# Kernel optimization log

Hardware: AMD Instinct MI355X
Metric: run time of the kernel (lower is better)

Reference implementation:

```python
import jax, jax.numpy as jnp
import numpy as np

SR = 16000; NFFT = 1024; HOP = 256; NMELS = 80; GRUH = 256; ZDIM = 16
NBINS = 65; HID = 512; B = 8; TLEN = 160000; PAD = NFFT // 2; IRLEN = 8000

def _consts():
    freqs = np.linspace(0, SR / 2, NFFT // 2 + 1); fsq = freqs ** 2
    aw = (12194.217 ** 2 * fsq ** 2) / ((fsq + 20.6 ** 2) * (fsq + 107.7 ** 2) * (fsq + 737.9 ** 2) * (fsq + 12194.217 ** 2) ** 0.5 + 1e-8)
    h2m = lambda f: 2595.0 * np.log10(1.0 + f / 700.0)
    m2h = lambda m: 700.0 * (10.0 ** (m / 2595.0) - 1.0)
    f_pts = m2h(np.linspace(h2m(0.0), h2m(SR / 2.0), NMELS + 2))
    fd = f_pts[1:] - f_pts[:-1]
    sl = f_pts[None, :] - freqs[:, None]
    fb = np.maximum(0.0, np.minimum(-sl[:, :-2] / fd[:-1], sl[:, 2:] / fd[1:]))
    win = 0.5 - 0.5 * np.cos(2.0 * np.pi * np.arange(NFFT) / NFFT)  # periodic hann
    return jnp.asarray(aw, jnp.float32), jnp.asarray(fb, jnp.float32), jnp.asarray(win, jnp.float32)
AW, MELFB, WIN = _consts()

def _frame(x, size, hop):
    n = (x.shape[-1] - size) // hop + 1
    idx = jnp.arange(n)[:, None] * hop + jnp.arange(size)[None, :]
    return x[:, idx]

def _stft(x):  # [B,T] -> [B, n_frames, 513] complex
    xp = jnp.pad(x, ((0, 0), (PAD, PAD)), mode='reflect')
    return jnp.fft.rfft(_frame(xp, NFFT, HOP) * WIN, axis=-1)

def _istft(spec, length):  # [B, n_frames, 513] -> [B, length]
    fr = jnp.fft.irfft(spec, n=NFFT, axis=-1) * WIN
    n = fr.shape[1]; total = (n - 1) * HOP + NFFT
    idx = (jnp.arange(n)[:, None] * HOP + jnp.arange(NFFT)[None, :]).reshape(-1)
    out = jnp.zeros((fr.shape[0], total), fr.dtype).at[:, idx].add(fr.reshape(fr.shape[0], -1))
    wsq = jnp.zeros((total,), WIN.dtype).at[idx].add(jnp.tile(WIN ** 2, (n,)))
    out = out / jnp.where(wsq > 1e-11, wsq, 1.0)
    return out[:, PAD:PAD + length]

def _lin_interp(x, size):  # torch F.interpolate(mode='linear', align_corners=False) on last axis
    L = x.shape[-1]
    pos = jnp.clip((jnp.arange(size) + 0.5) * (L / size) - 0.5, 0.0, L - 1.0)
    lo = jnp.floor(pos).astype(jnp.int32); hi = jnp.minimum(lo + 1, L - 1); w = pos - lo
    return x[..., lo] * (1.0 - w) + x[..., hi] * w

def _gru(x, wih, whh, bih, bhh):  # torch nn.GRU, batch_first, h0=0
    xp = x @ wih.T + bih
    def step(h, xt):
        gh = h @ whh.T + bhh
        xr, xz, xn = jnp.split(xt, 3, -1); hr, hz, hn = jnp.split(gh, 3, -1)
        r = jax.nn.sigmoid(xr + hr); z = jax.nn.sigmoid(xz + hz)
        nn_ = jnp.tanh(xn + r * hn)
        h = (1.0 - z) * nn_ + z * h
        return h, h
    h0 = jnp.zeros((x.shape[0], whh.shape[1]), x.dtype)
    _, hs = jax.lax.scan(step, h0, jnp.swapaxes(xp, 0, 1))
    return jnp.swapaxes(hs, 0, 1)

def _forward(audio, gender, age, gru_wih, gru_whh, gru_bih, gru_bhh, proj_w, proj_b,
             w0, b0, g0, e0, w1, b1, g1, e1, w2, b2, g2, e2,
             oq_w, oq_b, vt_w, vt_b, nf_w, nf_b, ir):
    # --- pitch via autocorrelation ---
    xp = jnp.pad(audio, ((0, 0), (PAD, PAD)), mode='reflect')
    fr = _frame(xp, NFFT, HOP)
    ps = jnp.abs(jnp.fft.rfft(fr, n=2 * NFFT, axis=-1)) ** 2
    ac = jnp.fft.irfft(ps, n=2 * NFFT, axis=-1)[..., :NFFT]
    ac = ac / (ac[..., :1] + 1e-8)
    min_lag, max_lag = SR // 1000, SR // 50  # 16, 320
    reg = ac[..., min_lag:max_lag]
    mv = jnp.max(reg, -1); mi = jnp.argmax(reg, -1)
    f0 = SR / (mi.astype(jnp.float32) + min_lag + 1e-8)
    f0 = jnp.where(mv < 0.3, 0.0, f0)[..., None]  # [B,F,1]
    # --- loudness + mels ---
    spec = jnp.abs(_stft(audio)) ** 2  # [B,F,513]
    loud = 10.0 * jnp.log10(jnp.mean((spec + 1e-8) * AW, -1, keepdims=True))  # [B,F,1]
    mels = jnp.log(spec @ MELFB + 1e-5)  # [B,F,80]
    mels = (mels - mels.mean(1, keepdims=True)) / jnp.sqrt(mels.var(1, keepdims=True) + 1e-5)
    z = _gru(mels, gru_wih, gru_whh, gru_bih, gru_bhh) @ proj_w.T + proj_b  # [B,F,16]
    Fn = f0.shape[1]
    # --- controller ---
    gb = jnp.broadcast_to(gender[:, None, :], (gender.shape[0], Fn, 2))
    ab = jnp.broadcast_to(age[:, None, :], (age.shape[0], Fn, 1))
    h = jnp.concatenate([z, (jnp.log(f0 + 1e-5) - 4.0) / 4.0, loud / 100.0 + 1.0, gb, ab], -1)
    for W, bb, gm, bt in ((w0, b0, g0, e0), (w1, b1, g1, e1), (w2, b2, g2, e2)):
        h = h @ W.T + bb
        h = (h - h.mean(-1, keepdims=True)) / jnp.sqrt(h.var(-1, keepdims=True) + 1e-5) * gm + bt
        h = jnp.where(h >= 0, h, 0.1 * h)  # LeakyReLU(0.1)
    oq = jax.nn.sigmoid(h @ oq_w.T + oq_b)
    vt = jax.nn.sigmoid(h @ vt_w.T + vt_b)
    nf = jax.nn.sigmoid(h @ nf_w.T + nf_b)
    amp = 10.0 ** (loud / 20.0)
    # --- decoder ---
    L = audio.shape[-1]
    f0u = _lin_interp(f0[..., 0], L); ampu = _lin_interp(amp[..., 0], L); oqu = _lin_interp(oq[..., 0], L)
    phase = jnp.cumsum(f0u / SR, -1); p = phase - jnp.floor(phase)
    oqc = jnp.clip(oqu, 0.1, 0.9)
    pulse = 0.5 * (1.0 - jnp.cos(jnp.pi * p / (oqc + 1e-8)))
    g = pulse * jax.nn.sigmoid((oqc - p) * 100.0)
    glottal = jnp.pad(g[..., 1:] - g[..., :-1], ((0, 0), (1, 0)))
    noise = jax.random.normal(jax.random.key(42), glottal.shape, glottal.dtype)
    def apply_filter(ex, filt):
        es = _stft(ex)  # [B,nf,513]
        ft = _lin_interp(jnp.swapaxes(filt, 1, 2), es.shape[1])  # time interp
        ff = _lin_interp(jnp.swapaxes(ft, 1, 2), es.shape[2])    # bin interp 65->513
        return _istft(es * ff, L)
    dry = (apply_filter(glottal, vt) + apply_filter(noise, nf)) * ampu
    # --- FFT reverb ---
    nconv = int(2 ** int(np.ceil(np.log2(L + IRLEN - 1))))
    wet = jnp.fft.irfft(jnp.fft.rfft(dry, n=nconv) * jnp.fft.rfft(ir, n=nconv), n=nconv)[..., :L]
    return wet, dry

def setup_inputs() -> dict:
    ks = iter(jax.random.split(jax.random.key(0), 48))
    def nrm(shape, s=0.05):
        return jax.random.normal(next(ks), shape, jnp.float32) * s
    inp = {}
    inp['audio'] = jax.random.normal(next(ks), (B, TLEN), jnp.float32)
    inp['gender'] = jax.random.uniform(next(ks), (B, 2), jnp.float32)
    inp['age'] = jax.random.uniform(next(ks), (B, 1), jnp.float32)
    inp['gru_wih'] = nrm((3 * GRUH, NMELS)); inp['gru_whh'] = nrm((3 * GRUH, GRUH))
    inp['gru_bih'] = jnp.zeros((3 * GRUH,), jnp.float32); inp['gru_bhh'] = jnp.zeros((3 * GRUH,), jnp.float32)
    inp['proj_w'] = nrm((ZDIM, GRUH)); inp['proj_b'] = jnp.zeros((ZDIM,), jnp.float32)
    din = ZDIM + 5
    inp['w0'] = nrm((HID, din)); inp['b0'] = jnp.zeros((HID,), jnp.float32)
    inp['g0'] = jnp.ones((HID,), jnp.float32); inp['e0'] = jnp.zeros((HID,), jnp.float32)
    inp['w1'] = nrm((HID, HID)); inp['b1'] = jnp.zeros((HID,), jnp.float32)
    inp['g1'] = jnp.ones((HID,), jnp.float32); inp['e1'] = jnp.zeros((HID,), jnp.float32)
    inp['w2'] = nrm((HID, HID)); inp['b2'] = jnp.zeros((HID,), jnp.float32)
    inp['g2'] = jnp.ones((HID,), jnp.float32); inp['e2'] = jnp.zeros((HID,), jnp.float32)
    inp['oq_w'] = nrm((1, HID)); inp['oq_b'] = jnp.zeros((1,), jnp.float32)
    inp['vt_w'] = nrm((NBINS, HID)); inp['vt_b'] = jnp.zeros((NBINS,), jnp.float32)
    inp['nf_w'] = nrm((NBINS, HID)); inp['nf_b'] = jnp.zeros((NBINS,), jnp.float32)
    decay = jnp.exp(-jnp.linspace(0.0, 5.0, IRLEN))
    inp['ir'] = jax.random.normal(next(ks), (IRLEN,), jnp.float32) * 0.1 * decay
    return inp

def reference(audio, gender, age, gru_wih, gru_whh, gru_bih, gru_bhh, proj_w, proj_b,
              w0, b0, g0, e0, w1, b1, g1, e1, w2, b2, g2, e2,
              oq_w, oq_b, vt_w, vt_b, nf_w, nf_b, ir):
    return _forward(audio, gender, age, gru_wih, gru_whh, gru_bih, gru_bhh, proj_w, proj_b,
                    w0, b0, g0, e0, w1, b1, g1, e1, w2, b2, g2, e2,
                    oq_w, oq_b, vt_w, vt_b, nf_w, nf_b, ir)
```

## Files before the change

### kernel.cpp

```cpp
#include <hip/hip_runtime.h>
#include <math.h>

#define SRF 16000.0f
#define HOP 256
#define FRM 626
#define BB 8
#define TLEN 160000
#define NFRM (BB*FRM)
#define NCONV 262144
#define ACCLEN 161024
#define GCH 40

constexpr size_t oWIN   = 0;
constexpr size_t oTW    = oWIN + 1024;
constexpr size_t oDIAG  = oTW + 1024;
constexpr size_t oTWF   = oDIAG + 16;
constexpr size_t oTWC   = oTWF + 1024;
constexpr size_t oAW    = oTWC + 1024;
constexpr size_t oMELFB = oAW + 513;
constexpr size_t oWSQI  = oMELFB + 513*80;
constexpr size_t oWIHT  = oWSQI + ACCLEN;
constexpr size_t oW0T   = oWIHT + 80*768;
constexpr size_t oW1T   = oW0T + 21*512;
constexpr size_t oW2T   = oW1T + 512*512;
constexpr size_t oVTT   = oW2T + 512*512;
constexpr size_t oNFT   = oVTT + 512*65;
constexpr size_t oF0    = oNFT + 512*65;
constexpr size_t oLOUD  = oF0 + NFRM;
constexpr size_t oOQ    = oLOUD + NFRM;
constexpr size_t oVT    = oOQ + NFRM;
constexpr size_t oNF    = oVT + (size_t)NFRM*65;
constexpr size_t oGLOT  = oNF + (size_t)NFRM*65;
constexpr size_t oNOISE = oGLOT + (size_t)BB*TLEN;
constexpr size_t oACC   = oNOISE + (size_t)BB*TLEN;
constexpr size_t oCONVA = oACC + (size_t)BB*ACCLEN;
constexpr size_t oEND   = oCONVA + (size_t)5*NCONV*2;
constexpr size_t oXP    = oEND;
constexpr size_t oGSUM  = oXP + (size_t)FRM*768*8;
constexpr size_t oGPRE  = oGSUM + 320;
constexpr size_t oEND2  = oGPRE + 640;
constexpr size_t oCONVB = oWSQI;
constexpr size_t oMEL = oCONVA;
constexpr size_t oHS  = oMEL + (size_t)NFRM*80;

constexpr long R_WIN=1024, R_TW=512, R_TWF=512, R_TWC=512, R_AW=513, R_MELFB=41040,
  R_WSQI=161024, R_WIHT=61440, R_W0T=10752, R_W1T=262144, R_W2T=262144,
  R_VTT=33280, R_NFT=33280, R_IR=NCONV;
constexpr long INIT_TOTAL = R_WIN+R_TW+R_TWF+R_TWC+R_AW+R_MELFB+R_WSQI+R_WIHT+R_W0T+
  R_W1T+R_W2T+R_VTT+R_NFT+R_IR;

constexpr int NOISEB = 313;
constexpr int ZACCB  = 315;
constexpr int MEGA_BLOCKS = 1 + NFRM + NOISEB + ZACCB;

typedef float f32x4 __attribute__((ext_vector_type(4)));
typedef __bf16 bf16x8 __attribute__((ext_vector_type(8)));
typedef short short8 __attribute__((ext_vector_type(8)));
#define MFMA_BF16 __builtin_amdgcn_mfma_f32_16x16x32_bf16

__device__ inline int mirror_idx(int j) {
  if (j < 0) j = -j;
  if (j >= TLEN) j = 2*TLEN - 2 - j;
  return j;
}
__device__ inline float sigm(float x) { return 1.0f/(1.0f + expf(-x)); }
__device__ inline unsigned short f2bf(float x) {
  unsigned u = __float_as_uint(x);
  return (unsigned short)((u + 0x7FFFu + ((u >> 16) & 1u)) >> 16);
}
__device__ inline float tanh_fast(float x) {
  return 1.0f - 2.0f/(__expf(2.0f*x) + 1.0f);
}

__device__ inline float interpF(const float* v, int i) {
  float pos = ((float)i + 0.5f) * (626.0f/160000.0f) - 0.5f;
  pos = fminf(fmaxf(pos, 0.0f), 625.0f);
  int lo = (int)floorf(pos);
  int hi = min(lo + 1, 625);
  float w = pos - (float)lo;
  return v[lo]*(1.0f - w) + v[hi]*w;
}
__device__ inline float interp65(const float* v, int k) {
  float pos = ((float)k + 0.5f) * (65.0f/513.0f) - 0.5f;
  pos = fminf(fmaxf(pos, 0.0f), 64.0f);
  int lo = (int)floorf(pos);
  int hi = min(lo + 1, 64);
  float w = pos - (float)lo;
  return v[lo]*(1.0f - w) + v[hi]*w;
}
__device__ inline float gwave(float ph, float oqu) {
  float p = ph - floorf(ph);
  float oqc = fminf(fmaxf(oqu, 0.1f), 0.9f);
  float pulse = 0.5f*(1.0f - cosf(3.14159265358979f * p / (oqc + 1e-8f)));
  float gs = 1.0f/(1.0f + __expf(-(oqc - p)*100.0f));
  return pulse*gs;
}

template<int LOGN, int TS>
__device__ inline void fft2(float2* c, const float2* tw, int tid, int nthr, bool inv) {
  constexpr int N = 1 << LOGN;
  for (int s = 1; s <= LOGN; ++s) {
    const int half = 1 << (s-1);
    const int tstep = (N >> s) * TS;
    for (int bf = tid; bf < (N>>1); bf += nthr) {
      int jj = bf & (half-1);
      int i0 = ((bf >> (s-1)) << s) + jj;
      int i1 = i0 + half;
      float2 wv = tw[jj*tstep];
      float wi = inv ? -wv.y : wv.y;
      float2 u = c[i0], v = c[i1];
      float tr  = v.x*wv.x - v.y*wi;
      float tci = v.x*wi  + v.y*wv.x;
      c[i0] = make_float2(u.x + tr, u.y + tci);
      c[i1] = make_float2(u.x - tr, u.y - tci);
    }
    __syncthreads();
  }
}

__device__ inline void threefry2x32(unsigned k0, unsigned k1, unsigned x0, unsigned x1,
                                    unsigned& o0, unsigned& o1) {
  unsigned ks2 = k0 ^ k1 ^ 0x1BD11BDAu;
  x0 += k0; x1 += k1;
#define TF_R(r) { x0 += x1; x1 = (x1<<(r)) | (x1>>(32-(r))); x1 ^= x0; }
  TF_R(13) TF_R(15) TF_R(26) TF_R(6)
  x0 += k1; x1 += ks2 + 1u;
  TF_R(17) TF_R(29) TF_R(16) TF_R(24)
  x0 += ks2; x1 += k0 + 2u;
  TF_R(13) TF_R(15) TF_R(26) TF_R(6)
  x0 += k0; x1 += k1 + 3u;
  TF_R(17) TF_R(29) TF_R(16) TF_R(24)
  x0 += k1; x1 += ks2 + 4u;
  TF_R(13) TF_R(15) TF_R(26) TF_R(6)
  x0 += ks2; x1 += k0 + 5u;
#undef TF_R
  o0 = x0; o1 = x1;
}

__device__ inline float erfinv_f(float x) {
  float w = -log1pf(-x*x);
  float p;
  if (w < 5.0f) {
    w = w - 2.5f;
    p = 2.81022636e-08f;
    p = fmaf(p, w, 3.43273939e-07f);
    p = fmaf(p, w, -3.5233877e-06f);
    p = fmaf(p, w, -4.39150654e-06f);
    p = fmaf(p, w, 0.00021858087f);
    p = fmaf(p, w, -0.00125372503f);
    p = fmaf(p, w, -0.00417768164f);
    p = fmaf(p, w, 0.246640727f);
    p = fmaf(p, w, 1.50140941f);
  } else {
    w = sqrtf(w) - 3.0f;
    p = -0.000200214257f;
    p = fmaf(p, w, 0.000100950558f);
    p = fmaf(p, w, 0.00134934322f);
    p = fmaf(p, w, -0.00367342844f);
    p = fmaf(p, w, 0.00573950773f);
    p = fmaf(p, w, -0.0076224613f);
    p = fmaf(p, w, 0.00943887047f);
    p = fmaf(p, w, 1.00167406f);
    p = fmaf(p, w, 2.83297682f);
  }
  return p*x;
}
__device__ inline float normal_from_bits(unsigned bits) {
  float f = __uint_as_float((bits >> 9) | 0x3F800000u) - 1.0f;
  float x = fmaxf(-0.99999994f, fmaf(f, 1.99999994f, -0.99999994f));
  return 1.41421356237f * erfinv_f(x);
}

__device__ inline double mel_fpt(int j) {
  double mmax = 2595.0 * log10(1.0 + 8000.0/700.0);
  return 700.0 * (pow(10.0, (mmax * (double)j / 81.0) / 2595.0) - 1.0);
}

__global__ void k_init(float* W, const float* wih, const float* w0,
                       const float* w1, const float* w2, const float* vtw, const float* nfw,
                       const float* ir) {
  long id = (long)blockIdx.x*256 + threadIdx.x;
  if (id < R_WIN) {
    double w = 0.5 - 0.5*cos(2.0*M_PI*(double)id/1024.0);
    W[oWIN+id] = (float)w; return;
  } id -= R_WIN;
  if (id < R_TW) {
    double a = -2.0*M_PI*(double)id/1024.0;
    W[oTW+2*id] = (float)cos(a); W[oTW+2*id+1] = (float)sin(a); return;
  } id -= R_TW;
  if (id < R_TWF) {
    double a = -2.0*M_PI*(double)id/262144.0;
    W[oTWF+2*id] = (float)cos(a); W[oTWF+2*id+1] = (float)sin(a); return;
  } id -= R_TWF;
  if (id < R_TWC) {
    double a = -2.0*M_PI*(double)id/512.0;
    W[oTWC+2*id] = (float)cos(a); W[oTWC+2*id+1] = (float)sin(a); return;
  } id -= R_TWC;
  if (id < R_AW) {
    double fr = (double)id*(8000.0/512.0); double fsq = fr*fr;
    double num = 12194.217*12194.217*fsq*fsq;
    double den = (fsq+20.6*20.6)*(fsq+107.7*107.7)*(fsq+737.9*737.9)*sqrt(fsq+12194.217*12194.217) + 1e-8;
    W[oAW+id] = (float)(num/den); return;
  } id -= R_AW;
  if (id < R_MELFB) {
    int k = (int)(id/80), m = (int)(id%80);
    double fk = (double)k*(8000.0/512.0);
    double f0p = mel_fpt(m), f1p = mel_fpt(m+1), f2p = mel_fpt(m+2);
    double lower = (fk - f0p)/(f1p - f0p);
    double upper = (f2p - fk)/(f2p - f1p);
    double v = fmax(0.0, fmin(lower, upper));
    W[oMELFB+id] = (float)v; return;
  } id -= R_MELFB;
  if (id < R_WSQI) {
    int t = (int)id;
    int n1 = t/256; if (n1 > 625) n1 = 625;
    int n0t = t - 1023 + 255; int n0 = (n0t > 0) ? n0t/256 : 0;
    double s = 0.0;
    for (int n = n0; n <= n1; ++n) {
      int o = t - n*256;
      double wv = 0.5 - 0.5*cos(2.0*M_PI*(double)o/1024.0);
      s += wv*wv;
    }
    float sf = (float)s;
    W[oWSQI+t] = (sf > 1e-11f) ? (1.0f/sf) : 1.0f; return;
  } id -= R_WSQI;
  if (id < R_WIHT) { long k = id/768, g = id%768; W[oWIHT+id] = wih[g*80+k];  return; } id -= R_WIHT;
  if (id < R_W0T)  { long d = id/512, j = id%512; W[oW0T+id] = w0[j*21+d];   return; } id -= R_W0T;
  if (id < R_W1T)  { long k = id/512, j = id%512; W[oW1T+id] = w1[j*512+k];  return; } id -= R_W1T;
  if (id < R_W2T)  { long k = id/512, j = id%512; W[oW2T+id] = w2[j*512+k];  return; } id -= R_W2T;
  if (id < R_VTT)  { long k = id/65,  m = id%65;  W[oVTT+id] = vtw[m*512+k]; return; } id -= R_VTT;
  if (id < R_NFT)  { long k = id/65,  m = id%65;  W[oNFT+id] = nfw[m*512+k]; return; } id -= R_NFT;
  if (id < R_IR) {
    size_t base = oCONVA + 2*((size_t)4*NCONV + id);
    W[base] = (id < 8000) ? ir[id] : 0.0f; W[base+1] = 0.0f; return;
  }
}

__global__ __launch_bounds__(256) void k_stft_mel(const float* audio, float* W) {
  int blk = blockIdx.x; int b = blk/FRM, f = blk%FRM; int tid = threadIdx.x;
  __shared__ float2 cb[1024];
  __shared__ float spec[513];
  __shared__ float redbuf[4];
  const float* arow = audio + (size_t)b*TLEN;
  const float2* tw = (const float2*)(W + oTW);
  for (int i = tid; i < 1024; i += 256) {
    float v = arow[mirror_idx(f*256 + i - 512)] * W[oWIN + i];
    int pos = __brev((unsigned)i) >> 22;
    cb[pos] = make_float2(v, 0.f);
  }
  __syncthreads();
  fft2<10,1>(cb, tw, tid, 256, false);
  for (int k = tid; k < 513; k += 256) { float2 z = cb[k]; spec[k] = z.x*z.x + z.y*z.y; }
  __syncthreads();
  float part = 0.f;
  for (int k = tid; k < 513; k += 256) part += (spec[k] + 1e-8f) * W[oAW + k];
  for (int off = 32; off; off >>= 1) part += __shfl_down(part, off, 64);
  if ((tid & 63) == 0) redbuf[tid >> 6] = part;
  __syncthreads();
  if (tid == 0) {
    float s = redbuf[0]+redbuf[1]+redbuf[2]+redbuf[3];
    W[oLOUD + blk] = 10.0f * log10f(s / 513.0f);
  }
  for (int m = tid; m < 80; m += 256) {
    double f0p = mel_fpt(m), f2p = mel_fpt(m + 2);
    int klo = (int)(f0p * (512.0/8000.0)); if (klo < 0) klo = 0;
    int khi = (int)(f2p * (512.0/8000.0)) + 1; if (khi > 512) khi = 512;
    float s = 0.f;
    for (int k = klo; k <= khi; ++k) s += spec[k]*W[oMELFB + (size_t)k*80 + m];
    W[oMEL + (size_t)blk*80 + m] = logf(s + 1e-5f);
  }
}

__global__ void k_melnorm(float* W) {
  int id = blockIdx.x*256 + threadIdx.x;
  if (id >= BB*80) return;
  int b = id/80, m = id%80;
  double s = 0.0, ss = 0.0;
  for (int f = 0; f < FRM; ++f) {
    double v = W[oMEL + ((size_t)b*FRM + f)*80 + m];
    s += v; ss += v*v;
  }
  double mean = s/FRM;
  double var = ss/FRM - mean*mean;
  float mu = (float)mean;
  float rstd = (float)(1.0/sqrt(var + 1e-5));
  for (int f = 0; f < FRM; ++f) {
    size_t idx = oMEL + ((size_t)b*FRM + f)*80 + m;
    W[idx] = (W[idx] - mu)*rstd;
  }
}

__global__ void k_xp(float* W, const float* bih) {
  size_t id = (size_t)blockIdx.x*256 + threadIdx.x;
  if (id >= (size_t)FRM*768*8) return;
  int b = (int)(id & 7);
  int g = (int)((id >> 3) % 768);
  int t = (int)(id / (768*8));
  const float* mrow = W + oMEL + ((size_t)b*FRM + t)*80;
  float acc = bih[g];
  for (int k = 0; k < 80; ++k) acc = fmaf(mrow[k], W[oWIHT + (size_t)k*768 + g], acc);
  W[oXP + id] = acc;
}

__global__ __launch_bounds__(512, 2) void k_mega(float* W, const float* audio,
                                                 const float* whh, const float* bhh) {
  __shared__ unsigned short sB[32768];
  __shared__ unsigned short sA[4096];
  __shared__ float sGT[9216];
  __shared__ float fr4[4][1032];
  __shared__ float wpow[8];
  __shared__ float wmax[8];
  __shared__ int   wmaxi[8];
  int tid = threadIdx.x;
  int blk = blockIdx.x;

  if (blk == 0) {
    int w = tid >> 6, l = tid & 63;
    const float* XP = W + oXP;
    float* HS = W + oHS;

    for (int idx = tid; idx < 32768; idx += 512) {
      int lcol = idx >> 8, k = idx & 255;
      int gcol = 96*(lcol >> 4) + 80 + (lcol & 15);
      sB[lcol*256 + (k ^ ((lcol & 7) << 3))] = f2bf(whh[(size_t)gcol*256 + k]);
    }
    for (int idx = tid; idx < 4096; idx += 512) sA[idx] = 0;

    int cl = l & 15, khalf = (l >> 4) * 8;
    bf16x8 bw[40];
    #pragma unroll
    for (int t2 = 0; t2 < 5; ++t2) {
      int col = 96*w + 16*t2 + cl;
      #pragma unroll
      for (int kk = 0; kk < 8; ++kk) {
        const float* src = whh + (size_t)col*256 + kk*32 + khalf;
        short8 tmp;
        #pragma unroll
        for (int j = 0; j < 8; ++j) tmp[j] = (short)f2bf(src[j]);
        bw[t2*8 + kk] = __builtin_bit_cast(bf16x8, tmp);
      }
    }

    int g = tid & 255, bbase = tid >> 8;
    float bh_r = bhh[g], bh_z = bhh[256 + g], bh_n = bhh[512 + g];
    float hprev[4] = {0.f, 0.f, 0.f, 0.f};
    int aXor = (cl & 7) << 3;
    int lcol5 = w*16 + cl;
    int rowg = l >> 4;
    int colb = 96*w + cl;
    int gtw = colb*12 + rowg*4;
    size_t xpr = (size_t)g*8 + 4*bbase;
    size_t xpz = (size_t)(256 + g)*8 + 4*bbase;
    size_t xpn = (size_t)(512 + g)*8 + 4*bbase;
    int gtr0 = g*12 + 4*bbase;
    int gtr1 = (256 + g)*12 + 4*bbase;
    int gtr2 = (512 + g)*12 + 4*bbase;

    __syncthreads();

#define LDA(kk) (*(const bf16x8*)&sA[(cl)*256 + (((kk)*32 + khalf) ^ aXor)])
#define LDB(kk) (*(const bf16x8*)&sB[(lcol5)*256 + (((kk)*32 + khalf) ^ aXor)])
#define STEPK(A_, kk) \
      c0 = MFMA_BF16(A_, bw[0*8+(kk)], c0, 0, 0, 0); \
      c1 = MFMA_BF16(A_, bw[1*8+(kk)], c1, 0, 0, 0); \
      c2 = MFMA_BF16(A_, bw[2*8+(kk)], c2, 0, 0, 0); \
      c3 = MFMA_BF16(A_, bw[3*8+(kk)], c3, 0, 0, 0); \
      c4 = MFMA_BF16(A_, bw[4*8+(kk)], c4, 0, 0, 0); \
      c5 = MFMA_BF16(A_, LDB(kk), c5, 0, 0, 0);

    for (int t = 0; t < FRM; ++t) {
      size_t xbase = (size_t)t*6144;
      float4 xr4 = *(const float4*)&XP[xbase + xpr];
      float4 xz4 = *(const float4*)&XP[xbase + xpz];
      float4 xn4 = *(const float4*)&XP[xbase + xpn];
      f32x4 c0 = {0,0,0,0}, c1 = {0,0,0,0}, c2 = {0,0,0,0};
      f32x4 c3 = {0,0,0,0}, c4 = {0,0,0,0}, c5 = {0,0,0,0};
      bf16x8 a0 = LDA(0), a1 = LDA(1), a2 = LDA(2), a3 = LDA(3);
      STEPK(a0, 0) STEPK(a1, 1) STEPK(a2, 2) STEPK(a3, 3)
      a0 = LDA(4); a1 = LDA(5); a2 = LDA(6); a3 = LDA(7);
      STEPK(a0, 4) STEPK(a1, 5) STEPK(a2, 6) STEPK(a3, 7)
      if (rowg < 3) {
        *(f32x4*)&sGT[gtw + 0*192]  = c0;
        *(f32x4*)&sGT[gtw + 1*192]  = c1;
        *(f32x4*)&sGT[gtw + 2*192]  = c2;
        *(f32x4*)&sGT[gtw + 3*192]  = c3;
        *(f32x4*)&sGT[gtw + 4*192]  = c4;
        *(f32x4*)&sGT[gtw + 5*192]  = c5;
      }
      __syncthreads();
      f32x4 rv = *(const f32x4*)&sGT[gtr0];
      f32x4 zv = *(const f32x4*)&sGT[gtr1];
      f32x4 nv = *(const f32x4*)&sGT[gtr2];
      #pragma unroll
      for (int j = 0; j < 4; ++j) {
        int bb = 4*bbase + j;
        float r = 1.0f/(1.0f + __expf(-(xr4[j] + rv[j] + bh_r)));
        float z = 1.0f/(1.0f + __expf(-(xz4[j] + zv[j] + bh_z)));
        float nn = tanh_fast(xn4[j] + r*(nv[j] + bh_n));
        float h = (1.0f - z)*nn + z*hprev[j];
        hprev[j] = h;
        HS[((size_t)bb*FRM + t)*256 + g] = h;
        sA[bb*256 + (g ^ ((bb & 7) << 3))] = f2bf(h);
      }
      __syncthreads();
    }
#undef LDA
#undef LDB
#undef STEPK
    return;
  }
  blk -= 1;

  if (blk < NFRM) {
    int b = blk/FRM, f = blk%FRM;
    const float* arow = audio + (size_t)b*TLEN;
    for (int idx = tid; idx < 4*1032; idx += 512) {
      int s = idx/1032, i = idx - s*1032;
      int j = i + s;
      fr4[s][i] = (j < 1024) ? arow[mirror_idx(f*256 + j - 512)] : 0.f;
    }
    __syncthreads();
    int lane = tid & 63, wv = tid >> 6;
    float p = 0.f;
    for (int i = tid; i < 1024; i += 512) { float x = fr4[0][i]; p += x*x; }
    for (int off = 32; off; off >>= 1) p += __shfl_down(p, off, 64);
    if (lane == 0) wpow[wv] = p;
    float vbest = -1e30f; int ibest = tid;
    if (tid < 304) {
      int lag = 16 + tid;
      int s = lag & 3, base = lag - s;
      int qmax = (1023 - lag) >> 2;
      float acc = 0.f;
      for (int q = 0; q <= qmax; ++q) {
        float4 u = *(const float4*)&fr4[0][4*q];
        float4 v = *(const float4*)&fr4[s][base + 4*q];
        acc += u.x*v.x + u.y*v.y + u.z*v.z + u.w*v.w;
      }
      vbest = acc;
    }
    for (int off = 32; off; off >>= 1) {
      float v2 = __shfl_down(vbest, off, 64);
      int i2 = __shfl_down(ibest, off, 64);
      if (v2 > vbest || (v2 == vbest && i2 < ibest)) { vbest = v2; ibest = i2; }
    }
    if (lane == 0) { wmax[wv] = vbest; wmaxi[wv] = ibest; }
    __syncthreads();
    if (tid == 0) {
      float ac0 = 0.f;
      #pragma unroll
      for (int q = 0; q < 8; ++q) ac0 += wpow[q];
      float bv = wmax[0]; int bi = wmaxi[0];
      #pragma unroll
      for (int q = 1; q < 8; ++q) {
        if (wmax[q] > bv || (wmax[q] == bv && wmaxi[q] < bi)) { bv = wmax[q]; bi = wmaxi[q]; }
      }
      float inv = 1.0f/(ac0 + 1e-8f);
      float best = bv*inv;
      W[oF0 + (size_t)blk] = (best < 0.3f) ? 0.0f : (SRF/(float)(bi + 16));
    }
    return;
  }
  blk -= NFRM;

  if (blk < NOISEB) {
    size_t base = (size_t)blk*4096;
    #pragma unroll
    for (int j = 0; j < 8; ++j) {
      size_t p = base + (size_t)j*512 + tid;
      if (p < (size_t)BB*TLEN) {
        unsigned o0, o1;
        threefry2x32(0u, 42u, 0u, (unsigned)p, o0, o1);
        W[oNOISE + p] = normal_from_bits(o0 ^ o1);
      }
    }
    return;
  }
  blk -= NOISEB;

  {
    size_t base = (size_t)blk*4096;
    #pragma unroll
    for (int j = 0; j < 8; ++j) {
      size_t p = base + (size_t)j*512 + tid;
      if (p < (size_t)BB*ACCLEN) W[oACC + p] = 0.0f;
    }
  }
}

__device__ inline void ln_lrelu(float acc[8], float gj, float ej, float out[8][512],
                                float wred[8][8][2], float stat[8][2],
                                int tid, int lane, int wv, int j) {
  #pragma unroll
  for (int i = 0; i < 8; ++i) {
    float s = acc[i], ss = acc[i]*acc[i];
    for (int off = 32; off; off >>= 1) { s += __shfl_down(s, off, 64); ss += __shfl_down(ss, off, 64); }
    if (lane == 0) { wred[i][wv][0] = s; wred[i][wv][1] = ss; }
  }
  __syncthreads();
  if (tid < 8) {
    float s = 0.f, ss = 0.f;
    #pragma unroll
    for (int w = 0; w < 8; ++w) { s += wred[tid][w][0]; ss += wred[tid][w][1]; }
    float mean = s/512.0f;
    float var = ss/512.0f - mean*mean;
    stat[tid][0] = mean;
    stat[tid][1] = 1.0f/sqrtf(var + 1e-5f);
  }
  __syncthreads();
  #pragma unroll
  for (int i = 0; i < 8; ++i) {
    float v = (acc[i] - stat[i][0])*stat[i][1]*gj + ej;
    out[i][j] = (v >= 0.f) ? v : 0.1f*v;
  }
}

__global__ __launch_bounds__(512) void k_mlp(float* W, const float* gender, const float* age,
    const float* projw, const float* projb,
    const float* b0, const float* g0, const float* e0,
    const float* b1, const float* g1, const float* e1,
    const float* b2, const float* g2, const float* e2,
    const float* oqw, const float* oqb, const float* vtb, const float* nfb) {
  __shared__ float hbuf[8][256];
  __shared__ float in0[8][21];
  __shared__ float actA[8][512];
  __shared__ float actB[8][512];
  __shared__ float wred[8][8][2];
  __shared__ float stat[8][2];
  int tid = threadIdx.x; int q0 = blockIdx.x*8;
  for (int x = tid; x < 2048; x += 512) {
    int i = x >> 8, k = x & 255;
    hbuf[i][k] = W[oHS + ((size_t)(q0 + i))*256 + k];
  }
  __syncthreads();
  if (tid < 128) {
    int i = tid >> 4, zi = tid & 15;
    float a = projb[zi];
    for (int k = 0; k < 256; ++k) a = fmaf(hbuf[i][k], projw[zi*256 + k], a);
    in0[i][zi] = a;
  } else if (tid < 168) {
    int x = tid - 128; int i = x/5, d = 16 + x%5;
    int q = q0 + i; int b = q/FRM;
    float v;
    if (d == 16) v = (logf(W[oF0 + q] + 1e-5f) - 4.0f)*0.25f;
    else if (d == 17) v = W[oLOUD + q]/100.0f + 1.0f;
    else if (d == 18) v = gender[b*2];
    else if (d == 19) v = gender[b*2 + 1];
    else v = age[b];
    in0[i][d] = v;
  }
  __syncthreads();
  int j = tid, lane = tid & 63, wv = tid >> 6;
  float acc[8];
  #pragma unroll
  for (int i = 0; i < 8; ++i) acc[i] = b0[j];
  for (int d = 0; d < 21; ++d) {
    float w = W[oW0T + (size_t)d*512 + j];
    #pragma unroll
    for (int i = 0; i < 8; ++i) acc[i] = fmaf(in0[i][d], w, acc[i]);
  }
  ln_lrelu(acc, g0[j], e0[j], actA, wred, stat, tid, lane, wv, j);
  __syncthreads();
  #pragma unroll
  for (int i = 0; i < 8; ++i) acc[i] = b1[j];
  for (int k = 0; k < 512; ++k) {
    float w = W[oW1T + (size_t)k*512 + j];
    #pragma unroll
    for (int i = 0; i < 8; ++i) acc[i] = fmaf(actA[i][k], w, acc[i]);
  }
  ln_lrelu(acc, g1[j], e1[j], actB, wred, stat, tid, lane, wv, j);
  __syncthreads();
  #pragma unroll
  for (int i = 0; i < 8; ++i) acc[i] = b2[j];
  for (int k = 0; k < 512; ++k) {
    float w = W[oW2T + (size_t)k*512 + j];
    #pragma unroll
    for (int i = 0; i < 8; ++i) acc[i] = fmaf(actB[i][k], w, acc[i]);
  }
  ln_lrelu(acc, g2[j], e2[j], actA, wred, stat, tid, lane, wv, j);
  __syncthreads();
  for (int x = tid; x < 520; x += 512) {
    int i = x/65, m = x%65;
    float a = vtb[m], a2 = nfb[m];
    for (int k = 0; k < 512; ++k) {
      float h = actA[i][k];
      a  = fmaf(h, W[oVTT + (size_t)k*65 + m], a);
      a2 = fmaf(h, W[oNFT + (size_t)k*65 + m], a2);
    }
    W[oVT + (size_t)(q0+i)*65 + m] = sigm(a);
    W[oNF + (size_t)(q0+i)*65 + m] = sigm(a2);
  }
  if (tid < 8) {
    float a = oqb[0];
    for (int k = 0; k < 512; ++k) a = fmaf(actA[tid][k], oqw[k], a);
    W[oOQ + q0 + tid] = sigm(a);
  }
}

__global__ __launch_bounds__(256) void k_gsum(float* W) {
  int blk = blockIdx.x; int b = blk/GCH, c = blk%GCH; int tid = threadIdx.x;
  __shared__ float ws[4];
  const float* f0r = W + oF0 + (size_t)b*FRM;
  int i0 = c*4096 + tid*16;
  float s = 0.f;
  #pragma unroll
  for (int j = 0; j < 16; ++j) {
    int i = i0 + j;
    if (i < TLEN) s += interpF(f0r, i)*(1.0f/SRF);
  }
  for (int off = 32; off; off >>= 1) s += __shfl_down(s, off, 64);
  if ((tid & 63) == 0) ws[tid >> 6] = s;
  __syncthreads();
  if (tid == 0) W[oGSUM + (size_t)b*GCH + c] = ws[0]+ws[1]+ws[2]+ws[3];
}

__global__ void k_gscan(float* W) {
  if (blockIdx.x == 0 && threadIdx.x == 0) {
    double* P = (double*)(W + oGPRE);
    for (int b = 0; b < BB; ++b) {
      double a = 0.0;
      for (int c = 0; c < GCH; ++c) {
        P[b*GCH + c] = a;
        a += (double)W[oGSUM + (size_t)b*GCH + c];
      }
    }
  }
}

__global__ __launch_bounds__(256) void k_gapply(float* W) {
  int blk = blockIdx.x; int b = blk/GCH, c = blk%GCH; int tid = threadIdx.x;
  __shared__ float wss[4];
  __shared__ float lastw[4];
  const float* f0r = W + oF0 + (size_t)b*FRM;
  const float* oqr = W + oOQ + (size_t)b*FRM;
  float* grow = W + oGLOT + (size_t)b*TLEN;
  double P = ((const double*)(W + oGPRE))[b*GCH + c];
  int i0 = c*4096 + tid*16;
  int lane = tid & 63, wv = tid >> 6;
  float v[16]; float ts = 0.f;
  #pragma unroll
  for (int j = 0; j < 16; ++j) {
    int i = i0 + j;
    float x = (i < TLEN) ? interpF(f0r, i)*(1.0f/SRF) : 0.f;
    v[j] = x; ts += x;
  }
  float sc = ts;
  #pragma unroll
  for (int off = 1; off < 64; off <<= 1) {
    float o = __shfl_up(sc, off, 64);
    if (lane >= off) sc += o;
  }
  if (lane == 63) wss[wv] = sc;
  __syncthreads();
  float wpre = 0.f;
  for (int q = 0; q < wv; ++q) wpre += wss[q];
  double ph0 = P + (double)(wpre + sc - ts);
  float run = 0.f; float gq[16];
  #pragma unroll
  for (int j = 0; j < 16; ++j) {
    int i = i0 + j;
    run += v[j];
    float ph = (float)(ph0 + (double)run);
    gq[j] = gwave(ph, interpF(oqr, min(i, TLEN-1)));
  }
  float prev = __shfl_up(gq[15], 1, 64);
  if (lane == 63) lastw[wv] = gq[15];
  __syncthreads();
  if (lane == 0) {
    if (wv > 0) prev = lastw[wv - 1];
    else if (i0 > 0) prev = gwave((float)P, interpF(oqr, i0 - 1));
    else prev = 0.f;
  }
  #pragma unroll
  for (int j = 0; j < 16; ++j) {
    int i = i0 + j;
    if (i < TLEN) {
      float gl = (j == 0) ? prev : gq[j-1];
      grow[i] = (i == 0) ? 0.f : (gq[j] - gl);
    }
  }
}

__global__ __launch_bounds__(256) void k_filtsynth(float* W) {
  int blk = blockIdx.x; int b = blk/FRM, f = blk%FRM; int tid = threadIdx.x;
  __shared__ float2 cZ[1024], cS[1024];
  __shared__ float fvt[65], fnf[65];
  const float* grow = W + oGLOT + (size_t)b*TLEN;
  const float* nrow = W + oNOISE + (size_t)b*TLEN;
  const float2* tw = (const float2*)(W + oTW);
  for (int i = tid; i < 1024; i += 256) {
    int si = mirror_idx(f*256 + i - 512);
    float wv = W[oWIN + i];
    int pos = __brev((unsigned)i) >> 22;
    cZ[pos] = make_float2(grow[si]*wv, nrow[si]*wv);
  }
  if (tid < 65) {
    fvt[tid] = W[oVT + ((size_t)b*FRM + f)*65 + tid];
    fnf[tid] = W[oNF + ((size_t)b*FRM + f)*65 + tid];
  }
  __syncthreads();
  fft2<10,1>(cZ, tw, tid, 256, false);
  for (int k = tid; k <= 512; k += 256) {
    int km = (1024 - k) & 1023;
    float2 z1 = cZ[k], z2 = cZ[km];
    float Gr = 0.5f*(z1.x + z2.x), Gi = 0.5f*(z1.y - z2.y);
    float Nr = 0.5f*(z1.y + z2.y), Ni = 0.5f*(z2.x - z1.x);
    float fv = interp65(fvt, k), fn = interp65(fnf, k);
    float Sr = Gr*fv + Nr*fn, Si = Gi*fv + Ni*fn;
    cS[__brev((unsigned)k) >> 22] = make_float2(Sr, Si);
    if (km != k) cS[__brev((unsigned)km) >> 22] = make_float2(Sr, -Si);
  }
  __syncthreads();
  fft2<10,1>(cS, tw, tid, 256, true);
  float* arow = W + oACC + (size_t)b*ACCLEN + (size_t)f*256;
  for (int i = tid; i < 1024; i += 256) {
    float xv = cS[i].x*(1.0f/1024.0f)*W[oWIN + i];
    atomicAdd(arow + i, xv);
  }
}

__global__ void k_dry(float* W, float* dout) {
  size_t id = (size_t)blockIdx.x*256 + threadIdx.x;
  if (id >= (size_t)4*NCONV) return;
  int t = (int)(id / NCONV);
  int n = (int)(id % NCONV);
  float dv0 = 0.f, dv1 = 0.f;
  if (n < TLEN) {
    float pos = ((float)n + 0.5f) * (626.0f/160000.0f) - 0.5f;
    pos = fminf(fmaxf(pos, 0.0f), 625.0f);
    int lo = (int)floorf(pos);
    int hi = min(lo + 1, 625);
    float wgt = pos - (float)lo;
    float wsq = W[oWSQI + 512 + n];
    #pragma unroll
    for (int q = 0; q < 2; ++q) {
      int b = 2*t + q;
      float val = W[oACC + (size_t)b*ACCLEN + 512 + n] * wsq;
      const float* lrow = W + oLOUD + (size_t)b*FRM;
      float a0 = exp10f(lrow[lo]*0.05f);
      float a1 = exp10f(lrow[hi]*0.05f);
      float dv = val*(a0*(1.0f - wgt) + a1*wgt);
      if (q == 0) dv0 = dv; else dv1 = dv;
      dout[(size_t)BB*TLEN + (size_t)b*TLEN + n] = dv;
    }
  }
  ((float2*)(W + oCONVA))[id] = make_float2(dv0, dv1);
}

__global__ __launch_bounds__(256) void k_conv_f1(const float* in, float* out,
                                                 const float* tw, const float* twf,
                                                 const float* twc) {
  int blk = blockIdx.x; int t = blk >> 9; int bcol = blk & 511; int tid = threadIdx.x;
  __shared__ float2 cb[512];
  const float2* src = (const float2*)in + (size_t)t*NCONV;
  for (int a = tid; a < 512; a += 256) {
    int pos = __brev((unsigned)a) >> 23;
    cb[pos] = src[(size_t)a*512 + bcol];
  }
  __syncthreads();
  fft2<9,2>(cb, (const float2*)tw, tid, 256, false);
  float2* dst = (float2*)out + (size_t)t*NCONV + (size_t)bcol*512;
  for (int k1 = tid; k1 < 512; k1 += 256) {
    unsigned m = (unsigned)bcol * (unsigned)k1;
    float2 tc = ((const float2*)twc)[m >> 9];
    float2 tf = ((const float2*)twf)[m & 511];
    float wr = tc.x*tf.x - tc.y*tf.y;
    float wi = tc.x*tf.y + tc.y*tf.x;
    float2 v = cb[k1];
    dst[k1] = make_float2(v.x*wr - v.y*wi, v.x*wi + v.y*wr);
  }
}

__global__ __launch_bounds__(256) void k_conv_f2(const float* in, float* out, const float* tw) {
  int blk = blockIdx.x; int t = blk >> 9; int k1 = blk & 511; int tid = threadIdx.x;
  __shared__ float2 cb[512];
  const float2* src = (const float2*)in + (size_t)t*NCONV;
  for (int bb2 = tid; bb2 < 512; bb2 += 256) {
    int pos = __brev((unsigned)bb2) >> 23;
    cb[pos] = src[(size_t)bb2*512 + k1];
  }
  __syncthreads();
  fft2<9,2>(cb, (const float2*)tw, tid, 256, false);
  float2* dst = (float2*)out + (size_t)t*NCONV;
  for (int k2 = tid; k2 < 512; k2 += 256) {
    dst[(size_t)k1 + 512*(size_t)k2] = cb[k2];
  }
}

__global__ __launch_bounds__(256) void k_conv_f2w(const float* in, float* dout, const float* tw) {
  int blk = blockIdx.x; int t = blk >> 9; int k1 = blk & 511; int tid = threadIdx.x;
  __shared__ float2 cb[512];
  const float2* src = (const float2*)in + (size_t)t*NCONV;
  for (int bb2 = tid; bb2 < 512; bb2 += 256) {
    int pos = __brev((unsigned)bb2) >> 23;
    cb[pos] = src[(size_t)bb2*512 + k1];
  }
  __syncthreads();
  fft2<9,2>(cb, (const float2*)tw, tid, 256, false);
  float* d0 = dout + (size_t)(2*t)*TLEN;
  float* d1 = dout + (size_t)(2*t + 1)*TLEN;
  for (int k2 = tid; k2 < 512; k2 += 256) {
    int n = k1 + 512*k2;
    if (n < TLEN) {
      float2 V = cb[k2];
      d0[n] = V.x * (1.0f/262144.0f);
      d1[n] = -V.y * (1.0f/262144.0f);
    }
  }
}

__global__ void k_mul(float* W) {
  constexpr size_t HALF = NCONV/2;
  size_t id = (size_t)blockIdx.x*256 + threadIdx.x;
  if (id >= (size_t)4*(HALF + 1)) return;
  int t = (int)(id / (HALF + 1));
  size_t k = id % (HALF + 1);
  size_t km = (NCONV - k) & (NCONV - 1);
  float2* A = (float2*)(W + oCONVA);
  float2 z1 = A[(size_t)t*NCONV + k];
  float2 z2 = A[(size_t)t*NCONV + km];
  float2 c  = A[(size_t)4*NCONV + k];
  float X0r = 0.5f*(z1.x + z2.x), X0i = 0.5f*(z1.y - z2.y);
  float X1r = 0.5f*(z1.y + z2.y), X1i = 0.5f*(z2.x - z1.x);
  float P0r = X0r*c.x - X0i*c.y, P0i = X0r*c.y + X0i*c.x;
  float P1r = X1r*c.x - X1i*c.y, P1i = X1r*c.y + X1i*c.x;
  A[(size_t)t*NCONV + k] = make_float2(P0r - P1i, -(P0i + P1r));
  if (km != k) {
    A[(size_t)t*NCONV + km] = make_float2(P0r + P1i, P0i - P1r);
  }
}

extern "C" void kernel_launch(void* const* d_in, const int* in_sizes, int n_in,
                              void* d_out, int out_size, void* d_ws, size_t ws_size,
                              hipStream_t stream) {
  (void)in_sizes; (void)n_in; (void)out_size; (void)ws_size;
  const float* audio  = (const float*)d_in[0];
  const float* gender = (const float*)d_in[1];
  const float* age    = (const float*)d_in[2];
  const float* wih    = (const float*)d_in[3];
  const float* whh    = (const float*)d_in[4];
  const float* bih    = (const float*)d_in[5];
  const float* bhh    = (const float*)d_in[6];
  const float* projw  = (const float*)d_in[7];
  const float* projb  = (const float*)d_in[8];
  const float* w0     = (const float*)d_in[9];
  const float* b0     = (const float*)d_in[10];
  const float* g0     = (const float*)d_in[11];
  const float* e0     = (const float*)d_in[12];
  const float* w1     = (const float*)d_in[13];
  const float* b1     = (const float*)d_in[14];
  const float* g1     = (const float*)d_in[15];
  const float* e1     = (const float*)d_in[16];
  const float* w2     = (const float*)d_in[17];
  const float* b2     = (const float*)d_in[18];
  const float* g2     = (const float*)d_in[19];
  const float* e2     = (const float*)d_in[20];
  const float* oqw    = (const float*)d_in[21];
  const float* oqb    = (const float*)d_in[22];
  const float* vtw    = (const float*)d_in[23];
  const float* vtb    = (const float*)d_in[24];
  const float* nfw    = (const float*)d_in[25];
  const float* nfb    = (const float*)d_in[26];
  const float* ir     = (const float*)d_in[27];
  float* W = (float*)d_ws;
  float* dout = (float*)d_out;

  k_init<<<(int)((INIT_TOTAL + 255)/256), 256, 0, stream>>>(W, wih, w0, w1, w2, vtw, nfw, ir);
  k_stft_mel<<<NFRM, 256, 0, stream>>>(audio, W);
  k_melnorm<<<3, 256, 0, stream>>>(W);
  k_xp<<<(int)(((size_t)FRM*768*8 + 255)/256), 256, 0, stream>>>(W, bih);
  k_mega<<<MEGA_BLOCKS, 512, 0, stream>>>(W, audio, whh, bhh);
  k_mlp<<<NFRM/8, 512, 0, stream>>>(W, gender, age, projw, projb,
                                    b0, g0, e0, b1, g1, e1, b2, g2, e2, oqw, oqb, vtb, nfb);
  k_gsum<<<BB*GCH, 256, 0, stream>>>(W);
  k_gscan<<<1, 64, 0, stream>>>(W);
  k_gapply<<<BB*GCH, 256, 0, stream>>>(W);
  k_filtsynth<<<NFRM, 256, 0, stream>>>(W);
  k_dry<<<(int)(((size_t)4*NCONV + 255)/256), 256, 0, stream>>>(W, dout);
  k_conv_f1<<<5*512, 256, 0, stream>>>(W + oCONVA, W + oCONVB, W + oTW, W + oTWF, W + oTWC);
  k_conv_f2<<<5*512, 256, 0, stream>>>(W + oCONVB, W + oCONVA, W + oTW);
  k_mul<<<(int)(((size_t)4*(NCONV/2 + 1) + 255)/256), 256, 0, stream>>>(W);
  k_conv_f1<<<4*512, 256, 0, stream>>>(W + oCONVA, W + oCONVB, W + oTW, W + oTWF, W + oTWC);
  k_conv_f2w<<<4*512, 256, 0, stream>>>(W + oCONVB, dout, W + oTW);
}
```

Baseline: 2.177 ms.

## Remap GRU hidden columns so gates compute in MFMA registers, double-buffer h

Reassigns the recurrent weight columns so each wave's MFMA accumulators hold matching r, z, n gate columns for two hidden units. The gate nonlinearities are then applied directly from registers instead of going through a shared gate-transpose buffer. The hidden state is double-buffered in LDS, which removes one of the two block barriers per time step. The aim is to shorten the serial per-step latency of the 626-step recurrence. In exchange, only half the lanes do gate math, and correctness depends on the new column-to-lane mapping matching the MFMA output layout.

```diff
diff --git a/kernel.cpp b/kernel.cpp
--- a/kernel.cpp
+++ b/kernel.cpp
@@ -305,8 +305,7 @@
 __global__ __launch_bounds__(512, 2) void k_mega(float* W, const float* audio,
                                                  const float* whh, const float* bhh) {
   __shared__ unsigned short sB[32768];
-  __shared__ unsigned short sA[4096];
-  __shared__ float sGT[9216];
+  __shared__ unsigned short sA[2][4096];
   __shared__ float fr4[4][1032];
   __shared__ float wpow[8];
   __shared__ float wmax[8];
@@ -321,44 +320,46 @@
 
     for (int idx = tid; idx < 32768; idx += 512) {
       int lcol = idx >> 8, k = idx & 255;
-      int gcol = 96*(lcol >> 4) + 80 + (lcol & 15);
+      int gcol = 512 + 32*(lcol >> 4) + 16 + (lcol & 15);
       sB[lcol*256 + (k ^ ((lcol & 7) << 3))] = f2bf(whh[(size_t)gcol*256 + k]);
     }
-    for (int idx = tid; idx < 4096; idx += 512) sA[idx] = 0;
+    for (int idx = tid; idx < 8192; idx += 512) ((unsigned short*)sA)[idx] = 0;
 
     int cl = l & 15, khalf = (l >> 4) * 8;
     bf16x8 bw[40];
-    #pragma unroll
-    for (int t2 = 0; t2 < 5; ++t2) {
-      int col = 96*w + 16*t2 + cl;
+    {
+      const int tbase[5] = {32*w, 32*w + 16, 256 + 32*w, 256 + 32*w + 16, 512 + 32*w};
       #pragma unroll
-      for (int kk = 0; kk < 8; ++kk) {
-        const float* src = whh + (size_t)col*256 + kk*32 + khalf;
-        short8 tmp;
+      for (int t2 = 0; t2 < 5; ++t2) {
+        int col = tbase[t2] + cl;
         #pragma unroll
-        for (int j = 0; j < 8; ++j) tmp[j] = (short)f2bf(src[j]);
-        bw[t2*8 + kk] = __builtin_bit_cast(bf16x8, tmp);
+        for (int kk = 0; kk < 8; ++kk) {
+          const float* src = whh + (size_t)col*256 + kk*32 + khalf;
+          short8 tmp;
+          #pragma unroll
+          for (int j = 0; j < 8; ++j) tmp[j] = (short)f2bf(src[j]);
+          bw[t2*8 + kk] = __builtin_bit_cast(bf16x8, tmp);
+        }
       }
     }
 
-    int g = tid & 255, bbase = tid >> 8;
-    float bh_r = bhh[g], bh_z = bhh[256 + g], bh_n = bhh[512 + g];
-    float hprev[4] = {0.f, 0.f, 0.f, 0.f};
     int aXor = (cl & 7) << 3;
     int lcol5 = w*16 + cl;
-    int rowg = l >> 4;
-    int colb = 96*w + cl;
-    int gtw = colb*12 + rowg*4;
-    size_t xpr = (size_t)g*8 + 4*bbase;
-    size_t xpz = (size_t)(256 + g)*8 + 4*bbase;
-    size_t xpn = (size_t)(512 + g)*8 + 4*bbase;
-    int gtr0 = g*12 + 4*bbase;
-    int gtr1 = (256 + g)*12 + 4*bbase;
-    int gtr2 = (512 + g)*12 + 4*bbase;
+    int rowhalf = l >> 4;
+    int g0 = 32*w + cl, g1 = g0 + 16;
+    float bhr0 = bhh[g0], bhr1 = bhh[g1];
+    float bhz0 = bhh[256 + g0], bhz1 = bhh[256 + g1];
+    float bhn0 = bhh[512 + g0], bhn1 = bhh[512 + g1];
+    float hp0[4] = {0.f,0.f,0.f,0.f}, hp1[4] = {0.f,0.f,0.f,0.f};
+    size_t xr0o = (size_t)g0*8 + 4*rowhalf, xr1o = (size_t)g1*8 + 4*rowhalf;
+    size_t xz0o = (size_t)(256+g0)*8 + 4*rowhalf, xz1o = (size_t)(256+g1)*8 + 4*rowhalf;
+    size_t xn0o = (size_t)(512+g0)*8 + 4*rowhalf, xn1o = (size_t)(512+g1)*8 + 4*rowhalf;
+    bool gateOK = (l < 32);
+    int cur = 0;
 
     __syncthreads();
 
-#define LDA(kk) (*(const bf16x8*)&sA[(cl)*256 + (((kk)*32 + khalf) ^ aXor)])
+#define LDA(kk) (*(const bf16x8*)&sA[cur][(cl)*256 + (((kk)*32 + khalf) ^ aXor)])
 #define LDB(kk) (*(const bf16x8*)&sB[(lcol5)*256 + (((kk)*32 + khalf) ^ aXor)])
 #define STEPK(A_, kk) \
       c0 = MFMA_BF16(A_, bw[0*8+(kk)], c0, 0, 0, 0); \
@@ -370,39 +371,49 @@
 
     for (int t = 0; t < FRM; ++t) {
       size_t xbase = (size_t)t*6144;
-      float4 xr4 = *(const float4*)&XP[xbase + xpr];
-      float4 xz4 = *(const float4*)&XP[xbase + xpz];
-      float4 xn4 = *(const float4*)&XP[xbase + xpn];
+      float4 xr0, xr1, xz0, xz1, xn0, xn1;
+      if (gateOK) {
+        xr0 = *(const float4*)&XP[xbase + xr0o];
+        xr1 = *(const float4*)&XP[xbase + xr1o];
+        xz0 = *(const float4*)&XP[xbase + xz0o];
+        xz1 = *(const float4*)&XP[xbase + xz1o];
+        xn0 = *(const float4*)&XP[xbase + xn0o];
+        xn1 = *(const float4*)&XP[xbase + xn1o];
+      }
       f32x4 c0 = {0,0,0,0}, c1 = {0,0,0,0}, c2 = {0,0,0,0};
       f32x4 c3 = {0,0,0,0}, c4 = {0,0,0,0}, c5 = {0,0,0,0};
       bf16x8 a0 = LDA(0), a1 = LDA(1), a2 = LDA(2), a3 = LDA(3);
       STEPK(a0, 0) STEPK(a1, 1) STEPK(a2, 2) STEPK(a3, 3)
       a0 = LDA(4); a1 = LDA(5); a2 = LDA(6); a3 = LDA(7);
       STEPK(a0, 4) STEPK(a1, 5) STEPK(a2, 6) STEPK(a3, 7)
-      if (rowg < 3) {
-        *(f32x4*)&sGT[gtw + 0*192]  = c0;
-        *(f32x4*)&sGT[gtw + 1*192]  = c1;
-        *(f32x4*)&sGT[gtw + 2*192]  = c2;
-        *(f32x4*)&sGT[gtw + 3*192]  = c3;
-        *(f32x4*)&sGT[gtw + 4*192]  = c4;
-        *(f32x4*)&sGT[gtw + 5*192]  = c5;
+      if (gateOK) {
+        unsigned short* sAn = sA[cur ^ 1];
+        #pragma unroll
+        for (int j = 0; j < 4; ++j) {
+          int bb = 4*rowhalf + j;
+          int sw = (bb & 7) << 3;
+          {
+            float r = 1.0f/(1.0f + __expf(-(xr0[j] + c0[j] + bhr0)));
+            float z = 1.0f/(1.0f + __expf(-(xz0[j] + c2[j] + bhz0)));
+            float nn = tanh_fast(xn0[j] + r*(c4[j] + bhn0));
+            float h = (1.0f - z)*nn + z*hp0[j];
+            hp0[j] = h;
+            HS[((size_t)bb*FRM + t)*256 + g0] = h;
+            sAn[bb*256 + (g0 ^ sw)] = f2bf(h);
+          }
+          {
+            float r = 1.0f/(1.0f + __expf(-(xr1[j] + c1[j] + bhr1)));
+            float z = 1.0f/(1.0f + __expf(-(xz1[j] + c3[j] + bhz1)));
+            float nn = tanh_fast(xn1[j] + r*(c5[j] + bhn1));
+            float h = (1.0f - z)*nn + z*hp1[j];
+            hp1[j] = h;
+            HS[((size_t)bb*FRM + t)*256 + g1] = h;
+            sAn[bb*256 + (g1 ^ sw)] = f2bf(h);
+          }
+        }
       }
       __syncthreads();
-      f32x4 rv = *(const f32x4*)&sGT[gtr0];
-      f32x4 zv = *(const f32x4*)&sGT[gtr1];
-      f32x4 nv = *(const f32x4*)&sGT[gtr2];
-      #pragma unroll
-      for (int j = 0; j < 4; ++j) {
-        int bb = 4*bbase + j;
-        float r = 1.0f/(1.0f + __expf(-(xr4[j] + rv[j] + bh_r)));
-        float z = 1.0f/(1.0f + __expf(-(xz4[j] + zv[j] + bh_z)));
-        float nn = tanh_fast(xn4[j] + r*(nv[j] + bh_n));
-        float h = (1.0f - z)*nn + z*hprev[j];
-        hprev[j] = h;
-        HS[((size_t)bb*FRM + t)*256 + g] = h;
-        sA[bb*256 + (g ^ ((bb & 7) << 3))] = f2bf(h);
-      }
-      __syncthreads();
+      cur ^= 1;
     }
 #undef LDA
 #undef LDB
```

Result: slower. 4.004 ms (+83.9%).
